# Kernel tuning notes

Hardware: AMD Instinct MI355X
Metric: run time of the kernel (lower is better)

## Reference

```python
import jax, jax.numpy as jnp
import numpy as np

N = 100000
E = 300000
D = 128
EPS = 1e-5


def sage_conv(x, edge_index, Wl, bl, Wr):
    # PyG SAGEConv: out = lin_l(mean_{j in N(i)} x_j) + lin_r(x_i)
    src, dst = edge_index[0], edge_index[1]
    n = x.shape[0]
    agg = jax.ops.segment_sum(x[src], dst, num_segments=n)            # [N, d]
    cnt = jax.ops.segment_sum(jnp.ones((src.shape[0],), x.dtype), dst, num_segments=n)
    mean = agg / jnp.maximum(cnt, 1.0)[:, None]
    return mean @ Wl.T + bl + x @ Wr.T


def setup_inputs() -> dict:
    key = jax.random.key(0)
    ks = jax.random.split(key, 16)
    s = 0.05
    inp = {
        "feat": jax.random.normal(ks[0], (N, D), jnp.float32),
        "e0": jax.random.randint(ks[1], (2, E), 0, N, jnp.int32),
        "e1": jax.random.randint(ks[2], (2, E), 0, N, jnp.int32),
        "e2": jax.random.randint(ks[3], (2, E), 0, N, jnp.int32),
    }
    # per-etype SAGEConv params (in=hidden=128)
    for i, k in zip(range(3), (ks[4], ks[5], ks[6])):
        ka, kb = jax.random.split(k)
        inp[f"Wl{i}"] = jax.random.normal(ka, (D, D), jnp.float32) * s
        inp[f"bl{i}"] = jnp.zeros((D,), jnp.float32)
        inp[f"Wr{i}"] = jax.random.normal(kb, (D, D), jnp.float32) * s
    ka, kb = jax.random.split(ks[7])
    inp["Wla"] = jax.random.normal(ka, (D, D), jnp.float32) * s
    inp["bla"] = jnp.zeros((D,), jnp.float32)
    inp["Wra"] = jax.random.normal(kb, (D, D), jnp.float32) * s
    ka, kb = jax.random.split(ks[8])
    inp["Wf"] = jax.random.normal(ka, (D, D), jnp.float32) * s
    inp["bf"] = jnp.zeros((D,), jnp.float32)
    inp["Wrf"] = jax.random.normal(kb, (D, D), jnp.float32) * s
    inp["gamma"] = jnp.ones((D,), jnp.float32)
    inp["beta"] = jnp.zeros((D,), jnp.float32)
    inp["wt"] = jnp.ones((3,), jnp.float32)
    return inp


def reference(feat, Wl0, bl0, Wr0, Wl1, bl1, Wr1, Wl2, bl2, Wr2,
              Wla, bla, Wra, Wf, bf, Wrf, gamma, beta, wt, e0, e1, e2):
    out0 = sage_conv(feat, e0, Wl0, bl0, Wr0)
    out1 = sage_conv(feat, e1, Wl1, bl1, Wr1)
    out2 = sage_conv(feat, e2, Wl2, bl2, Wr2)
    all_e = jnp.concatenate([e0, e1, e2], axis=1)   # [2, 3E]
    all_out = sage_conv(feat, all_e, Wla, bla, Wra)
    comb = wt[0] * out0 + wt[1] * out1 + wt[2] * out2 + all_out
    comb = jax.nn.relu(comb)
    # BatchNorm1d (training mode: batch stats over node dim, biased var)
    mu = jnp.mean(comb, axis=0)
    var = jnp.mean((comb - mu) ** 2, axis=0)
    comb = (comb - mu) * jax.lax.rsqrt(var + EPS) * gamma + beta
    # dropout p=0.0 -> identity
    return sage_conv(comb, all_e, Wf, bf, Wrf)
```

## Files before the change

kernel.cpp:

```cpp
#include <hip/hip_runtime.h>

#define NN 100000
#define NE 300000
#define DD 128
#define NBLKG 782
#define NBLKSEG 49

typedef short bf16x8 __attribute__((ext_vector_type(8)));
typedef float f32x4 __attribute__((ext_vector_type(4)));
typedef unsigned u32x4 __attribute__((ext_vector_type(4)));

__device__ __forceinline__ unsigned short f2b(float f) {
    union { float f; unsigned u; } c; c.f = f;
    unsigned u = c.u;
    return (unsigned short)((u + 0x7fffu + ((u >> 16) & 1u)) >> 16);
}
__device__ __forceinline__ float b2lo(unsigned u) {
    union { float f; unsigned u; } c; c.u = u << 16; return c.f;
}
__device__ __forceinline__ float b2hi(unsigned u) {
    union { float f; unsigned u; } c; c.u = u & 0xffff0000u; return c.f;
}
__device__ __forceinline__ unsigned pack2(float lo, float hi) {
    return (unsigned)f2b(lo) | ((unsigned)f2b(hi) << 16);
}

__global__ __launch_bounds__(256) void feat_to_bf16(
    const float* __restrict__ feat, unsigned short* __restrict__ fb) {
    int gid = blockIdx.x * 256 + threadIdx.x;
    if (gid >= NN * 16) return;
    const f32x4* f4 = (const f32x4*)feat;
    f32x4 a = __builtin_nontemporal_load(&f4[gid * 2]);
    f32x4 b = __builtin_nontemporal_load(&f4[gid * 2 + 1]);
    uint4 o;
    o.x = pack2(a.x, a.y); o.y = pack2(a.z, a.w);
    o.z = pack2(b.x, b.y); o.w = pack2(b.z, b.w);
    ((uint4*)fb)[gid] = o;
}

__global__ __launch_bounds__(256) void prep_weights(
    const float* __restrict__ Wl0, const float* __restrict__ bl0, const float* __restrict__ Wr0,
    const float* __restrict__ Wl1, const float* __restrict__ bl1, const float* __restrict__ Wr1,
    const float* __restrict__ Wl2, const float* __restrict__ bl2, const float* __restrict__ Wr2,
    const float* __restrict__ Wla, const float* __restrict__ bla, const float* __restrict__ Wra,
    const float* __restrict__ Wf,  const float* __restrict__ bfv, const float* __restrict__ Wrf,
    const float* __restrict__ wt,
    unsigned short* __restrict__ WcatB, float* __restrict__ bias1,
    unsigned short* __restrict__ W2catB, float* __restrict__ bias2) {
    int idx = blockIdx.x * 256 + threadIdx.x;
    float w0 = wt[0], w1 = wt[1], w2 = wt[2];
    if (idx < 81920) {
        int f = idx / 640, k = idx % 640;
        float v;
        if (k < 128)      v = w0 * Wl0[f * 128 + k];
        else if (k < 256) v = w1 * Wl1[f * 128 + (k - 128)];
        else if (k < 384) v = w2 * Wl2[f * 128 + (k - 256)];
        else if (k < 512) v = Wla[f * 128 + (k - 384)];
        else {
            int kk = k - 512;
            v = w0 * Wr0[f * 128 + kk] + w1 * Wr1[f * 128 + kk] +
                w2 * Wr2[f * 128 + kk] + Wra[f * 128 + kk];
        }
        WcatB[idx] = f2b(v);
    } else if (idx < 81920 + 32768) {
        int j = idx - 81920;
        int f = j >> 8, k = j & 255;
        W2catB[j] = f2b((k < 128) ? Wf[f * 128 + k] : Wrf[f * 128 + (k - 128)]);
    } else if (idx < 81920 + 32768 + 128) {
        int f = idx - (81920 + 32768);
        bias1[f] = w0 * bl0[f] + w1 * bl1[f] + w2 * bl2[f] + bla[f];
        bias2[f] = bfv[f];
    }
}

__global__ __launch_bounds__(256) void count_deg(
    const int* __restrict__ e0, const int* __restrict__ e1, const int* __restrict__ e2,
    int* __restrict__ deg) {
    int gid = blockIdx.x * 256 + threadIdx.x;
    if (gid >= 3 * NE) return;
    int t = (gid < NE) ? 0 : ((gid < 2 * NE) ? 1 : 2);
    int i = gid - t * NE;
    const int* ep = (t == 0) ? e0 : ((t == 1) ? e1 : e2);
    atomicAdd(&deg[t * NN + ep[NE + i]], 1);
}

__global__ __launch_bounds__(256) void scan_local(
    const int* __restrict__ deg, int* __restrict__ rowstart, int* __restrict__ bsum) {
    __shared__ int sc[256];
    int b = blockIdx.x, tid = threadIdx.x;
    int seg = b / NBLKSEG, blk = b % NBLKSEG;
    int g0 = seg * NN;
    int base = blk * 2048 + tid * 8;
    int vals[8]; int tsum = 0;
#pragma unroll
    for (int j = 0; j < 8; ++j) {
        int l = base + j;
        int d = (l < NN) ? deg[g0 + l] : 0;
        vals[j] = tsum; tsum += d;
    }
    sc[tid] = tsum;
    __syncthreads();
    for (int off = 1; off < 256; off <<= 1) {
        int v = (tid >= off) ? sc[tid - off] : 0;
        __syncthreads();
        sc[tid] += v;
        __syncthreads();
    }
    int excl = sc[tid] - tsum;
#pragma unroll
    for (int j = 0; j < 8; ++j) {
        int l = base + j;
        if (l < NN) rowstart[g0 + l] = excl + vals[j];
    }
    if (tid == 255) bsum[b] = sc[255];
}

__global__ void scan_bsum(int* __restrict__ bsum) {
    int tid = threadIdx.x;
    if (tid < 3) {
        int run = 0;
        for (int b = 0; b < NBLKSEG; ++b) {
            int idx = tid * NBLKSEG + b;
            int t = bsum[idx]; bsum[idx] = run; run += t;
        }
    }
}

__global__ __launch_bounds__(256) void scan_fix(
    int* __restrict__ rowstart, int* __restrict__ fillpos, const int* __restrict__ bsum) {
    int b = blockIdx.x, tid = threadIdx.x;
    int seg = b / NBLKSEG, blk = b % NBLKSEG;
    int g0 = seg * NN;
    int base = blk * 2048 + tid * 8;
    int off = bsum[b];
#pragma unroll
    for (int j = 0; j < 8; ++j) {
        int l = base + j;
        if (l < NN) {
            int r = rowstart[g0 + l] + off;
            rowstart[g0 + l] = r;
            fillpos[g0 + l] = r;
        }
    }
}

__global__ __launch_bounds__(256) void fill_csr(
    const int* __restrict__ e0, const int* __restrict__ e1, const int* __restrict__ e2,
    int* __restrict__ fillpos, int* __restrict__ csr) {
    int gid = blockIdx.x * 256 + threadIdx.x;
    if (gid >= 3 * NE) return;
    int t = (gid < NE) ? 0 : ((gid < 2 * NE) ? 1 : 2);
    int i = gid - t * NE;
    const int* ep = (t == 0) ? e0 : ((t == 1) ? e1 : e2);
    int src = ep[i], dst = ep[NE + i];
    int p = atomicAdd(&fillpos[t * NN + dst], 1);
    csr[t * NE + p] = src;
}

__global__ __launch_bounds__(256) void gather1(
    const unsigned short* __restrict__ featB,
    const int* __restrict__ deg, const int* __restrict__ rowstart, const int* __restrict__ csr,
    unsigned short* __restrict__ meanB) {
    int n = __builtin_amdgcn_readfirstlane((int)((blockIdx.x * 256 + threadIdx.x) >> 6));
    if (n >= NN) return;
    int lane = threadIdx.x & 63;
    int d0 = deg[n], d1 = deg[NN + n], d2 = deg[2 * NN + n];
    int r0 = rowstart[n], r1 = rowstart[NN + n], r2 = rowstart[2 * NN + n];
    int b1 = d0, b2 = d0 + d1, dall = b2 + d2;

    auto eidx = [&](int j) -> int {
        if (j < b1)      return r0 + j;
        else if (j < b2) return NE + r1 + (j - b1);
        else             return 2 * NE + r2 + (j - b2);
    };

    float p0 = 0.f, p1 = 0.f;
    float sA0 = 0.f, sA1 = 0.f;
    float sB0 = 0.f, sB1 = 0.f;

    unsigned f0 = 0, f1 = 0, f2 = 0, f3 = 0, f4 = 0;
    int i5 = 0, i6 = 0;
    {
        int i0 = 0, i1 = 0, i2 = 0, i3 = 0, i4 = 0;
        if (dall > 0) i0 = csr[eidx(0)];
        if (dall > 1) i1 = csr[eidx(1)];
        if (dall > 2) i2 = csr[eidx(2)];
        if (dall > 3) i3 = csr[eidx(3)];
        if (dall > 4) i4 = csr[eidx(4)];
        if (dall > 5) i5 = csr[eidx(5)];
        if (dall > 6) i6 = csr[eidx(6)];
        if (dall > 0) f0 = *((const unsigned*)(featB + (size_t)i0 * DD) + lane);
        if (dall > 1) f1 = *((const unsigned*)(featB + (size_t)i1 * DD) + lane);
        if (dall > 2) f2 = *((const unsigned*)(featB + (size_t)i2 * DD) + lane);
        if (dall > 3) f3 = *((const unsigned*)(featB + (size_t)i3 * DD) + lane);
        if (dall > 4) f4 = *((const unsigned*)(featB + (size_t)i4 * DD) + lane);
    }
    for (int j = 0; j <= dall; ++j) {
        if (j == b1)   { sA0 = p0; sA1 = p1; }
        if (j == b2)   { sB0 = p0; sB1 = p1; }
        if (j == dall) break;
        unsigned u = f0;
        f0 = f1; f1 = f2; f2 = f3; f3 = f4;
        if (j + 5 < dall) f4 = *((const unsigned*)(featB + (size_t)i5 * DD) + lane);
        i5 = i6;
        if (j + 7 < dall) i6 = csr[eidx(j + 7)];
        p0 += b2lo(u); p1 += b2hi(u);
    }

    float inv0 = 1.0f / fmaxf((float)d0, 1.0f);
    float inv1 = 1.0f / fmaxf((float)d1, 1.0f);
    float inv2 = 1.0f / fmaxf((float)d2, 1.0f);
    float inva = 1.0f / fmaxf((float)dall, 1.0f);
    float m10 = sB0 - sA0, m11 = sB1 - sA1;
    float m20 = p0 - sB0,  m21 = p1 - sB1;
    unsigned* outp = (unsigned*)(meanB + (size_t)n * 512) + lane;
    __builtin_nontemporal_store(pack2(sA0 * inv0, sA1 * inv0), outp);
    __builtin_nontemporal_store(pack2(m10 * inv1, m11 * inv1), outp + 64);
    __builtin_nontemporal_store(pack2(m20 * inv2, m21 * inv2), outp + 128);
    __builtin_nontemporal_store(pack2(p0 * inva,  p1 * inva),  outp + 192);
}

__global__ __launch_bounds__(256) void gemm1_tile(
    const unsigned short* __restrict__ meanB, const unsigned short* __restrict__ featB,
    const unsigned short* __restrict__ WcatB, const float* __restrict__ bias1,
    unsigned short* __restrict__ comb, float* __restrict__ partials) {
    __shared__ unsigned short ABs[65536 / 2];
    unsigned short* As = ABs;
    unsigned short* Bs = ABs + 16384;
    int tid = threadIdx.x;
    int wid = tid >> 6, lane = tid & 63;
    int quad = lane >> 4, m16 = lane & 15;
    int nb = blockIdx.x * 128;
    int mb = (wid & 1) * 64, fb = (wid >> 1) * 64;
    f32x4 acc[4][4];
#pragma unroll
    for (int mi = 0; mi < 4; ++mi)
#pragma unroll
        for (int fi = 0; fi < 4; ++fi) acc[mi][fi] = (f32x4){0.f, 0.f, 0.f, 0.f};

    for (int kc = 0; kc < 5; ++kc) {
        __syncthreads();
#pragma unroll
        for (int it = 0; it < 8; ++it) {
            int idx = it * 256 + tid;
            int row = idx >> 4, chunk = idx & 15;
            int s = chunk >> 2, q = chunk & 3;
            int gr = min(nb + row, NN - 1);
            u32x4 v = (kc < 4)
                ? __builtin_nontemporal_load((const u32x4*)(meanB + (size_t)gr * 512 + kc * 128 + chunk * 8))
                : *(const u32x4*)(featB + (size_t)gr * DD + chunk * 8);
            *(u32x4*)&As[(((s * 128 + row) * 4) + q) * 8] = v;
        }
#pragma unroll
        for (int it = 0; it < 8; ++it) {
            int idx = it * 256 + tid;
            int f = idx >> 4, chunk = idx & 15;
            int s = chunk >> 2, q = chunk & 3;
            u32x4 v = *(const u32x4*)(WcatB + (size_t)f * 640 + kc * 128 + chunk * 8);
            *(u32x4*)&Bs[(((s * 128 + f) * 4) + q) * 8] = v;
        }
        __syncthreads();
#pragma unroll
        for (int s = 0; s < 4; ++s) {
            bf16x8 av[4], bv[4];
#pragma unroll
            for (int mi = 0; mi < 4; ++mi)
                av[mi] = *(const bf16x8*)&As[(((s * 128 + mb + mi * 16 + m16) * 4) + quad) * 8];
#pragma unroll
            for (int fi = 0; fi < 4; ++fi)
                bv[fi] = *(const bf16x8*)&Bs[(((s * 128 + fb + fi * 16 + m16) * 4) + quad) * 8];
#pragma unroll
            for (int mi = 0; mi < 4; ++mi)
#pragma unroll
                for (int fi = 0; fi < 4; ++fi)
                    acc[mi][fi] = __builtin_amdgcn_mfma_f32_16x16x32_bf16(av[mi], bv[fi], acc[mi][fi], 0, 0, 0);
        }
    }
    __syncthreads();
    float* bnS = (float*)ABs;
    float* bnQ = bnS + 128;
    if (tid < 128) { bnS[tid] = 0.f; bnQ[tid] = 0.f; }
    __syncthreads();
#pragma unroll
    for (int fi = 0; fi < 4; ++fi) {
        int f = fb + fi * 16 + m16;
        float bb = bias1[f];
        float s = 0.f, q = 0.f;
#pragma unroll
        for (int mi = 0; mi < 4; ++mi) {
#pragma unroll
            for (int r = 0; r < 4; ++r) {
                int row = nb + mb + mi * 16 + quad * 4 + r;
                float v = fmaxf(acc[mi][fi][r] + bb, 0.f);
                if (row < NN) {
                    s += v; q += v * v;
                    comb[(size_t)row * DD + f] = f2b(v);
                }
            }
        }
        atomicAdd(&bnS[f], s);
        atomicAdd(&bnQ[f], q);
    }
    __syncthreads();
    if (tid < 128) {
        partials[(size_t)tid * NBLKG + blockIdx.x] = bnS[tid];
        partials[(size_t)(128 + tid) * NBLKG + blockIdx.x] = bnQ[tid];
    }
}

__global__ __launch_bounds__(256) void bnfin(
    const float* __restrict__ partials,
    const float* __restrict__ gamma, const float* __restrict__ beta,
    float* __restrict__ bnA, float* __restrict__ bnB) {
    __shared__ float rs[256], rq[256];
    int f = blockIdx.x, tid = threadIdx.x;
    float s = 0.f, q = 0.f;
    for (int r = tid; r < NBLKG; r += 256) {
        s += partials[(size_t)f * NBLKG + r];
        q += partials[(size_t)(128 + f) * NBLKG + r];
    }
    rs[tid] = s; rq[tid] = q;
    __syncthreads();
    for (int off = 128; off > 0; off >>= 1) {
        if (tid < off) { rs[tid] += rs[tid + off]; rq[tid] += rq[tid + off]; }
        __syncthreads();
    }
    if (tid == 0) {
        float mu = rs[0] / (float)NN;
        float var = fmaxf(rq[0] / (float)NN - mu * mu, 0.f);
        float a = gamma[f] * rsqrtf(var + 1e-5f);
        bnA[f] = a;
        bnB[f] = beta[f] - mu * a;
    }
}

__global__ __launch_bounds__(256) void gather2(
    const unsigned short* __restrict__ comb,
    const int* __restrict__ deg, const int* __restrict__ rowstart, const int* __restrict__ csr,
    const float* __restrict__ bnA, const float* __restrict__ bnB,
    unsigned short* __restrict__ meanC) {
    int n = __builtin_amdgcn_readfirstlane((int)((blockIdx.x * 256 + threadIdx.x) >> 6));
    if (n >= NN) return;
    int lane = threadIdx.x & 63;
    int d0 = deg[n], d1 = deg[NN + n], d2 = deg[2 * NN + n];
    int r0 = rowstart[n], r1 = rowstart[NN + n], r2 = rowstart[2 * NN + n];
    int b1 = d0, b2 = d0 + d1, dall = b2 + d2;

    auto eidx = [&](int j) -> int {
        if (j < b1)      return r0 + j;
        else if (j < b2) return NE + r1 + (j - b1);
        else             return 2 * NE + r2 + (j - b2);
    };

    float p0 = 0.f, p1 = 0.f;
    unsigned f0 = 0, f1 = 0, f2 = 0, f3 = 0, f4 = 0;
    int i5 = 0, i6 = 0;
    {
        int i0 = 0, i1 = 0, i2 = 0, i3 = 0, i4 = 0;
        if (dall > 0) i0 = csr[eidx(0)];
        if (dall > 1) i1 = csr[eidx(1)];
        if (dall > 2) i2 = csr[eidx(2)];
        if (dall > 3) i3 = csr[eidx(3)];
        if (dall > 4) i4 = csr[eidx(4)];
        if (dall > 5) i5 = csr[eidx(5)];
        if (dall > 6) i6 = csr[eidx(6)];
        if (dall > 0) f0 = *((const unsigned*)(comb + (size_t)i0 * DD) + lane);
        if (dall > 1) f1 = *((const unsigned*)(comb + (size_t)i1 * DD) + lane);
        if (dall > 2) f2 = *((const unsigned*)(comb + (size_t)i2 * DD) + lane);
        if (dall > 3) f3 = *((const unsigned*)(comb + (size_t)i3 * DD) + lane);
        if (dall > 4) f4 = *((const unsigned*)(comb + (size_t)i4 * DD) + lane);
    }
    for (int j = 0; j < dall; ++j) {
        unsigned u = f0;
        f0 = f1; f1 = f2; f2 = f3; f3 = f4;
        if (j + 5 < dall) f4 = *((const unsigned*)(comb + (size_t)i5 * DD) + lane);
        i5 = i6;
        if (j + 7 < dall) i6 = csr[eidx(j + 7)];
        p0 += b2lo(u); p1 += b2hi(u);
    }

    float v0 = 0.f, v1 = 0.f;
    if (dall > 0) {
        float inv = 1.0f / (float)dall;
        float2 a = *(const float2*)&bnA[lane * 2];
        float2 b = *(const float2*)&bnB[lane * 2];
        v0 = a.x * (p0 * inv) + b.x;
        v1 = a.y * (p1 * inv) + b.y;
    }
    __builtin_nontemporal_store(pack2(v0, v1),
                                (unsigned*)(meanC + (size_t)n * DD) + lane);
}

__global__ __launch_bounds__(256) void gemm2_tile(
    const unsigned short* __restrict__ meanC, const unsigned short* __restrict__ comb,
    const float* __restrict__ bnA, const float* __restrict__ bnB,
    const unsigned short* __restrict__ W2catB, const float* __restrict__ bias2,
    float* __restrict__ out) {
    __shared__ unsigned short ABs[65536 / 2];
    unsigned short* As = ABs;
    unsigned short* Bs = ABs + 16384;
    int tid = threadIdx.x;
    int wid = tid >> 6, lane = tid & 63;
    int quad = lane >> 4, m16 = lane & 15;
    int nb = blockIdx.x * 128;
    int mb = (wid & 1) * 64, fb = (wid >> 1) * 64;
    f32x4 acc[4][4];
#pragma unroll
    for (int mi = 0; mi < 4; ++mi)
#pragma unroll
        for (int fi = 0; fi < 4; ++fi) acc[mi][fi] = (f32x4){0.f, 0.f, 0.f, 0.f};

    for (int kc = 0; kc < 2; ++kc) {
        __syncthreads();
#pragma unroll
        for (int it = 0; it < 8; ++it) {
            int idx = it * 256 + tid;
            int row = idx >> 4, chunk = idx & 15;
            int s = chunk >> 2, q = chunk & 3;
            int gr = min(nb + row, NN - 1);
            u32x4 v;
            if (kc == 0) {
                v = __builtin_nontemporal_load((const u32x4*)(meanC + (size_t)gr * DD + chunk * 8));
            } else {
                u32x4 c4 = *(const u32x4*)(comb + (size_t)gr * DD + chunk * 8);
                int cb = chunk * 8;
                float4 a0 = *(const float4*)&bnA[cb], a1 = *(const float4*)&bnA[cb + 4];
                float4 b0 = *(const float4*)&bnB[cb], b1 = *(const float4*)&bnB[cb + 4];
                v.x = pack2(a0.x * b2lo(c4.x) + b0.x, a0.y * b2hi(c4.x) + b0.y);
                v.y = pack2(a0.z * b2lo(c4.y) + b0.z, a0.w * b2hi(c4.y) + b0.w);
                v.z = pack2(a1.x * b2lo(c4.z) + b1.x, a1.y * b2hi(c4.z) + b1.y);
                v.w = pack2(a1.z * b2lo(c4.w) + b1.z, a1.w * b2hi(c4.w) + b1.w);
            }
            *(u32x4*)&As[(((s * 128 + row) * 4) + q) * 8] = v;
        }
#pragma unroll
        for (int it = 0; it < 8; ++it) {
            int idx = it * 256 + tid;
            int f = idx >> 4, chunk = idx & 15;
            int s = chunk >> 2, q = chunk & 3;
            u32x4 v = *(const u32x4*)(W2catB + (size_t)f * 256 + kc * 128 + chunk * 8);
            *(u32x4*)&Bs[(((s * 128 + f) * 4) + q) * 8] = v;
        }
        __syncthreads();
#pragma unroll
        for (int s = 0; s < 4; ++s) {
            bf16x8 av[4], bv[4];
#pragma unroll
            for (int mi = 0; mi < 4; ++mi)
                av[mi] = *(const bf16x8*)&As[(((s * 128 + mb + mi * 16 + m16) * 4) + quad) * 8];
#pragma unroll
            for (int fi = 0; fi < 4; ++fi)
                bv[fi] = *(const bf16x8*)&Bs[(((s * 128 + fb + fi * 16 + m16) * 4) + quad) * 8];
#pragma unroll
            for (int mi = 0; mi < 4; ++mi)
#pragma unroll
                for (int fi = 0; fi < 4; ++fi)
                    acc[mi][fi] = __builtin_amdgcn_mfma_f32_16x16x32_bf16(av[mi], bv[fi], acc[mi][fi], 0, 0, 0);
        }
    }
#pragma unroll
    for (int fi = 0; fi < 4; ++fi) {
        int f = fb + fi * 16 + m16;
        float bb = bias2[f];
#pragma unroll
        for (int mi = 0; mi < 4; ++mi) {
#pragma unroll
            for (int r = 0; r < 4; ++r) {
                int row = nb + mb + mi * 16 + quad * 4 + r;
                if (row < NN)
                    __builtin_nontemporal_store(acc[mi][fi][r] + bb,
                                                &out[(size_t)row * DD + f]);
            }
        }
    }
}

extern "C" void kernel_launch(void* const* d_in, const int* in_sizes, int n_in,
                              void* d_out, int out_size, void* d_ws, size_t ws_size,
                              hipStream_t stream) {
    const float* feat = (const float*)d_in[0];
    const int* e0 = (const int*)d_in[1];
    const int* e1 = (const int*)d_in[2];
    const int* e2 = (const int*)d_in[3];
    const float* Wl0 = (const float*)d_in[4];
    const float* bl0 = (const float*)d_in[5];
    const float* Wr0 = (const float*)d_in[6];
    const float* Wl1 = (const float*)d_in[7];
    const float* bl1 = (const float*)d_in[8];
    const float* Wr1 = (const float*)d_in[9];
    const float* Wl2 = (const float*)d_in[10];
    const float* bl2 = (const float*)d_in[11];
    const float* Wr2 = (const float*)d_in[12];
    const float* Wla = (const float*)d_in[13];
    const float* bla = (const float*)d_in[14];
    const float* Wra = (const float*)d_in[15];
    const float* Wf  = (const float*)d_in[16];
    const float* bfv = (const float*)d_in[17];
    const float* Wrf = (const float*)d_in[18];
    const float* gamma = (const float*)d_in[19];
    const float* beta  = (const float*)d_in[20];
    const float* wt    = (const float*)d_in[21];

    int* deg      = (int*)d_ws;
    int* rowstart = deg + 3 * NN;
    int* fillpos  = rowstart + 3 * NN;
    int* csr      = fillpos + 3 * NN;
    int* bsum     = csr + 3 * NE;
    float* partials = (float*)(bsum + 160);
    float* bias1  = partials + 256 * NBLKG;
    float* bias2  = bias1 + 128;
    float* bnA    = bias2 + 128;
    float* bnB    = bnA + 128;
    unsigned short* WcatB  = (unsigned short*)(bnB + 128);
    unsigned short* W2catB = WcatB + 81920;
    unsigned short* comb   = W2catB + 32768;
    unsigned short* featB  = comb + (size_t)NN * DD;
    unsigned short* meanB  = featB + (size_t)NN * DD;
    unsigned short* meanC  = meanB + (size_t)NN * 512;

    hipMemsetAsync(deg, 0, (size_t)3 * NN * sizeof(int), stream);

    feat_to_bf16<<<6250, 256, 0, stream>>>(feat, featB);
    prep_weights<<<449, 256, 0, stream>>>(Wl0, bl0, Wr0, Wl1, bl1, Wr1, Wl2, bl2, Wr2,
                                          Wla, bla, Wra, Wf, bfv, Wrf, wt,
                                          WcatB, bias1, W2catB, bias2);
    count_deg<<<3516, 256, 0, stream>>>(e0, e1, e2, deg);
    scan_local<<<147, 256, 0, stream>>>(deg, rowstart, bsum);
    scan_bsum<<<1, 64, 0, stream>>>(bsum);
    scan_fix<<<147, 256, 0, stream>>>(rowstart, fillpos, bsum);
    fill_csr<<<3516, 256, 0, stream>>>(e0, e1, e2, fillpos, csr);

    gather1<<<25000, 256, 0, stream>>>(featB, deg, rowstart, csr, meanB);
    gemm1_tile<<<NBLKG, 256, 0, stream>>>(meanB, featB, WcatB, bias1, comb, partials);
    bnfin<<<128, 256, 0, stream>>>(partials, gamma, beta, bnA, bnB);
    gather2<<<25000, 256, 0, stream>>>(comb, deg, rowstart, csr, bnA, bnB, meanC);
    gemm2_tile<<<NBLKG, 256, 0, stream>>>(meanC, comb, bnA, bnB, W2catB, bias2,
                                          (float*)d_out);
}
```

Measured before the change: 460.5 us.

## Interleave per-etype CSR into one unified per-node CSR with combined degree

Rebuilds the CSR so that each node's neighbours from all three edge types sit contiguously, in etype order, in a single array. A unified row start and total degree are precomputed in scan_fix, so both gather kernels can read indices linearly from one pointer instead of resolving a three-way branch per edge. This removes the per-edge index selection and should give more contiguous index reads in the gathers. In exchange, scan_fix reads more arrays and writes extra rowstartU and degall arrays.

```diff
diff --git a/kernel.cpp b/kernel.cpp
--- a/kernel.cpp
+++ b/kernel.cpp
@@ -85,7 +85,7 @@
 }
 
 __global__ __launch_bounds__(256) void scan_local(
-    const int* __restrict__ deg, int* __restrict__ rowstart, int* __restrict__ bsum) {
+    const int* __restrict__ deg, int* __restrict__ rsloc, int* __restrict__ bsum) {
     __shared__ int sc[256];
     int b = blockIdx.x, tid = threadIdx.x;
     int seg = b / NBLKSEG, blk = b % NBLKSEG;
@@ -110,7 +110,7 @@
 #pragma unroll
     for (int j = 0; j < 8; ++j) {
         int l = base + j;
-        if (l < NN) rowstart[g0 + l] = excl + vals[j];
+        if (l < NN) rsloc[g0 + l] = excl + vals[j];
     }
     if (tid == 255) bsum[b] = sc[255];
 }
@@ -127,26 +127,29 @@
 }
 
 __global__ __launch_bounds__(256) void scan_fix(
-    int* __restrict__ rowstart, int* __restrict__ fillpos, const int* __restrict__ bsum) {
-    int b = blockIdx.x, tid = threadIdx.x;
-    int seg = b / NBLKSEG, blk = b % NBLKSEG;
-    int g0 = seg * NN;
+    const int* __restrict__ deg, const int* __restrict__ rsloc, const int* __restrict__ bsum,
+    int* __restrict__ fillpos, int* __restrict__ rowstartU, int* __restrict__ degall) {
+    int blk = blockIdx.x, tid = threadIdx.x;
     int base = blk * 2048 + tid * 8;
-    int off = bsum[b];
+    int o0 = bsum[blk], o1 = bsum[NBLKSEG + blk], o2 = bsum[2 * NBLKSEG + blk];
 #pragma unroll
     for (int j = 0; j < 8; ++j) {
         int l = base + j;
         if (l < NN) {
-            int r = rowstart[g0 + l] + off;
-            rowstart[g0 + l] = r;
-            fillpos[g0 + l] = r;
+            int d0 = deg[l], d1 = deg[NN + l], d2 = deg[2 * NN + l];
+            int rU = (rsloc[l] + o0) + (rsloc[NN + l] + o1) + (rsloc[2 * NN + l] + o2);
+            fillpos[l] = rU;
+            fillpos[NN + l] = rU + d0;
+            fillpos[2 * NN + l] = rU + d0 + d1;
+            rowstartU[l] = rU;
+            degall[l] = d0 + d1 + d2;
         }
     }
 }
 
 __global__ __launch_bounds__(256) void fill_csr(
     const int* __restrict__ e0, const int* __restrict__ e1, const int* __restrict__ e2,
-    int* __restrict__ fillpos, int* __restrict__ csr) {
+    int* __restrict__ fillpos, int* __restrict__ csrU) {
     int gid = blockIdx.x * 256 + threadIdx.x;
     if (gid >= 3 * NE) return;
     int t = (gid < NE) ? 0 : ((gid < 2 * NE) ? 1 : 2);
@@ -154,25 +157,21 @@
     const int* ep = (t == 0) ? e0 : ((t == 1) ? e1 : e2);
     int src = ep[i], dst = ep[NE + i];
     int p = atomicAdd(&fillpos[t * NN + dst], 1);
-    csr[t * NE + p] = src;
+    csrU[p] = src;
 }
 
 __global__ __launch_bounds__(256) void gather1(
     const unsigned short* __restrict__ featB,
-    const int* __restrict__ deg, const int* __restrict__ rowstart, const int* __restrict__ csr,
+    const int* __restrict__ deg, const int* __restrict__ rowstartU,
+    const int* __restrict__ degall, const int* __restrict__ csrU,
     unsigned short* __restrict__ meanB) {
     int n = __builtin_amdgcn_readfirstlane((int)((blockIdx.x * 256 + threadIdx.x) >> 6));
     if (n >= NN) return;
     int lane = threadIdx.x & 63;
-    int d0 = deg[n], d1 = deg[NN + n], d2 = deg[2 * NN + n];
-    int r0 = rowstart[n], r1 = rowstart[NN + n], r2 = rowstart[2 * NN + n];
-    int b1 = d0, b2 = d0 + d1, dall = b2 + d2;
-
-    auto eidx = [&](int j) -> int {
-        if (j < b1)      return r0 + j;
-        else if (j < b2) return NE + r1 + (j - b1);
-        else             return 2 * NE + r2 + (j - b2);
-    };
+    int d0 = deg[n], d1 = deg[NN + n];
+    int dall = degall[n];
+    int b1 = d0, b2 = d0 + d1;
+    const int* cp = csrU + rowstartU[n];
 
     float p0 = 0.f, p1 = 0.f;
     float sA0 = 0.f, sA1 = 0.f;
@@ -182,13 +181,13 @@
     int i5 = 0, i6 = 0;
     {
         int i0 = 0, i1 = 0, i2 = 0, i3 = 0, i4 = 0;
-        if (dall > 0) i0 = csr[eidx(0)];
-        if (dall > 1) i1 = csr[eidx(1)];
-        if (dall > 2) i2 = csr[eidx(2)];
-        if (dall > 3) i3 = csr[eidx(3)];
-        if (dall > 4) i4 = csr[eidx(4)];
-        if (dall > 5) i5 = csr[eidx(5)];
-        if (dall > 6) i6 = csr[eidx(6)];
+        if (dall > 0) i0 = cp[0];
+        if (dall > 1) i1 = cp[1];
+        if (dall > 2) i2 = cp[2];
+        if (dall > 3) i3 = cp[3];
+        if (dall > 4) i4 = cp[4];
+        if (dall > 5) i5 = cp[5];
+        if (dall > 6) i6 = cp[6];
         if (dall > 0) f0 = *((const unsigned*)(featB + (size_t)i0 * DD) + lane);
         if (dall > 1) f1 = *((const unsigned*)(featB + (size_t)i1 * DD) + lane);
         if (dall > 2) f2 = *((const unsigned*)(featB + (size_t)i2 * DD) + lane);
@@ -203,10 +202,11 @@
         f0 = f1; f1 = f2; f2 = f3; f3 = f4;
         if (j + 5 < dall) f4 = *((const unsigned*)(featB + (size_t)i5 * DD) + lane);
         i5 = i6;
-        if (j + 7 < dall) i6 = csr[eidx(j + 7)];
+        if (j + 7 < dall) i6 = cp[j + 7];
         p0 += b2lo(u); p1 += b2hi(u);
     }
 
+    int d2 = dall - b2;
     float inv0 = 1.0f / fmaxf((float)d0, 1.0f);
     float inv1 = 1.0f / fmaxf((float)d1, 1.0f);
     float inv2 = 1.0f / fmaxf((float)d2, 1.0f);
@@ -336,34 +336,28 @@
 
 __global__ __launch_bounds__(256) void gather2(
     const unsigned short* __restrict__ comb,
-    const int* __restrict__ deg, const int* __restrict__ rowstart, const int* __restrict__ csr,
+    const int* __restrict__ rowstartU, const int* __restrict__ degall,
+    const int* __restrict__ csrU,
     const float* __restrict__ bnA, const float* __restrict__ bnB,
     unsigned short* __restrict__ meanC) {
     int n = __builtin_amdgcn_readfirstlane((int)((blockIdx.x * 256 + threadIdx.x) >> 6));
     if (n >= NN) return;
     int lane = threadIdx.x & 63;
-    int d0 = deg[n], d1 = deg[NN + n], d2 = deg[2 * NN + n];
-    int r0 = rowstart[n], r1 = rowstart[NN + n], r2 = rowstart[2 * NN + n];
-    int b1 = d0, b2 = d0 + d1, dall = b2 + d2;
-
-    auto eidx = [&](int j) -> int {
-        if (j < b1)      return r0 + j;
-        else if (j < b2) return NE + r1 + (j - b1);
-        else             return 2 * NE + r2 + (j - b2);
-    };
+    int dall = degall[n];
+    const int* cp = csrU + rowstartU[n];
 
     float p0 = 0.f, p1 = 0.f;
     unsigned f0 = 0, f1 = 0, f2 = 0, f3 = 0, f4 = 0;
     int i5 = 0, i6 = 0;
     {
         int i0 = 0, i1 = 0, i2 = 0, i3 = 0, i4 = 0;
-        if (dall > 0) i0 = csr[eidx(0)];
-        if (dall > 1) i1 = csr[eidx(1)];
-        if (dall > 2) i2 = csr[eidx(2)];
-        if (dall > 3) i3 = csr[eidx(3)];
-        if (dall > 4) i4 = csr[eidx(4)];
-        if (dall > 5) i5 = csr[eidx(5)];
-        if (dall > 6) i6 = csr[eidx(6)];
+        if (dall > 0) i0 = cp[0];
+        if (dall > 1) i1 = cp[1];
+        if (dall > 2) i2 = cp[2];
+        if (dall > 3) i3 = cp[3];
+        if (dall > 4) i4 = cp[4];
+        if (dall > 5) i5 = cp[5];
+        if (dall > 6) i6 = cp[6];
         if (dall > 0) f0 = *((const unsigned*)(comb + (size_t)i0 * DD) + lane);
         if (dall > 1) f1 = *((const unsigned*)(comb + (size_t)i1 * DD) + lane);
         if (dall > 2) f2 = *((const unsigned*)(comb + (size_t)i2 * DD) + lane);
@@ -375,7 +369,7 @@
         f0 = f1; f1 = f2; f2 = f3; f3 = f4;
         if (j + 5 < dall) f4 = *((const unsigned*)(comb + (size_t)i5 * DD) + lane);
         i5 = i6;
-        if (j + 7 < dall) i6 = csr[eidx(j + 7)];
+        if (j + 7 < dall) i6 = cp[j + 7];
         p0 += b2lo(u); p1 += b2hi(u);
     }
 
@@ -502,11 +496,13 @@
     const float* wt    = (const float*)d_in[21];
 
     int* deg      = (int*)d_ws;
-    int* rowstart = deg + 3 * NN;
-    int* fillpos  = rowstart + 3 * NN;
-    int* csr      = fillpos + 3 * NN;
-    int* bsum     = csr + 3 * NE;
-    float* partials = (float*)(bsum + 160);
+    int* rsloc    = deg + 3 * NN;
+    int* fillpos  = rsloc + 3 * NN;
+    int* csrU     = fillpos + 3 * NN;
+    int* bsum     = csrU + 3 * NE;
+    int* rowstartU = bsum + 160;
+    int* degall    = rowstartU + NN;
+    float* partials = (float*)(degall + NN);
     float* bias1  = partials + 256 * NBLKG;
     float* bias2  = bias1 + 128;
     float* bnA    = bias2 + 128;
@@ -525,15 +521,15 @@
                                           Wla, bla, Wra, Wf, bfv, Wrf, wt,
                                           WcatB, bias1, W2catB, bias2);
     count_deg<<<3516, 256, 0, stream>>>(e0, e1, e2, deg);
-    scan_local<<<147, 256, 0, stream>>>(deg, rowstart, bsum);
+    scan_local<<<147, 256, 0, stream>>>(deg, rsloc, bsum);
     scan_bsum<<<1, 64, 0, stream>>>(bsum);
-    scan_fix<<<147, 256, 0, stream>>>(rowstart, fillpos, bsum);
-    fill_csr<<<3516, 256, 0, stream>>>(e0, e1, e2, fillpos, csr);
-
-    gather1<<<25000, 256, 0, stream>>>(featB, deg, rowstart, csr, meanB);
+    scan_fix<<<NBLKSEG, 256, 0, stream>>>(deg, rsloc, bsum, fillpos, rowstartU, degall);
+    fill_csr<<<3516, 256, 0, stream>>>(e0, e1, e2, fillpos, csrU);
+
+    gather1<<<25000, 256, 0, stream>>>(featB, deg, rowstartU, degall, csrU, meanB);
     gemm1_tile<<<NBLKG, 256, 0, stream>>>(meanB, featB, WcatB, bias1, comb, partials);
     bnfin<<<128, 256, 0, stream>>>(partials, gamma, beta, bnA, bnB);
-    gather2<<<25000, 256, 0, stream>>>(comb, deg, rowstart, csr, bnA, bnB, meanC);
+    gather2<<<25000, 256, 0, stream>>>(comb, rowstartU, degall, csrU, bnA, bnB, meanC);
     gemm2_tile<<<NBLKG, 256, 0, stream>>>(meanC, comb, bnA, bnB, W2catB, bias2,
                                           (float*)d_out);
 }
```

Measured after the change: 467.9 us. About the same (+1.6%).
